# Kernel tuning notes

Hardware: AMD Instinct MI355X
Metric: run time of the kernel (lower is better)

Reference implementation:

```python
import jax, jax.numpy as jnp
import numpy as np

BS, P, R, D = 32, 128, 16, 1024
RHO = 0.97
EPS = 1e-8


def unit_normalize(x):
    return x / jnp.maximum(jnp.linalg.norm(x, axis=-1, keepdims=True), EPS)


def setup_inputs() -> dict:
    key = jax.random.key(0)
    ks = jax.random.split(key, 12)
    scale = 1.0 / np.sqrt(D)
    return {
        "x_all": jax.random.normal(ks[0], (BS, P, D), jnp.float32),
        "h_all": jax.random.normal(ks[1], (BS, P, D), jnp.float32),
        "surprise_all": jax.random.uniform(ks[2], (BS, P, 1), jnp.float32) * 8.0,
        "reset_mask": jax.random.bernoulli(ks[3], 0.05, (BS, P)),
        "pm_K": unit_normalize(jax.random.normal(ks[4], (BS, R, D), jnp.float32)),
        "pm_V": unit_normalize(jax.random.normal(ks[5], (BS, R, D), jnp.float32)),
        "pm_a": jax.random.uniform(ks[6], (BS, R), jnp.float32),
        "elig_K0": jnp.zeros((BS, R, D), jnp.float32),
        "elig_V0": jnp.zeros((BS, R, D), jnp.float32),
        "W_k": jax.random.normal(ks[7], (D, D), jnp.float32) * scale,
        "b_k": jnp.zeros((D,), jnp.float32),
        "W_v": jax.random.normal(ks[8], (D, D), jnp.float32) * scale,
        "b_v": jnp.zeros((D,), jnp.float32),
    }


def reference(x_all, h_all, surprise_all, reset_mask, pm_K, pm_V, pm_a,
              elig_K0, elig_V0, W_k, b_k, W_v, b_v):
    # ---- apply_batch: read-only slot-memory readout over P tokens ----
    x_q = unit_normalize(x_all)                                  # [BS,P,D]
    scores = jnp.einsum('brd,bpd->bpr', pm_K, x_q)               # [BS,P,R]
    weighted = pm_a[:, None, :] * scores                         # [BS,P,R]
    y_pm = jnp.einsum('bpr,brd->bpd', weighted, pm_V)            # [BS,P,D]

    # ---- update_eligibility_batch: affine scan over P tokens ----
    k_cand = unit_normalize(jnp.einsum('bpd,de->bpe', x_all, W_k) + b_k)  # [BS,P,D]
    v_cand = jnp.einsum('bpd,de->bpe', h_all, W_v) + b_v                  # [BS,P,D]
    gate = jnp.clip(surprise_all[..., 0] / 5.0, 0.0, 1.0)                 # [BS,P]
    a_keep = RHO * (1.0 - reset_mask.astype(jnp.float32))                 # [BS,P]

    def step(carry, inp):
        eK, eV = carry                      # each [BS,R,D]
        k, v, g, a = inp                    # [BS,D],[BS,D],[BS],[BS]
        # b_t = gate * cand, broadcast across the R slots (matches torch expand)
        eK = a[:, None, None] * eK + (g[:, None] * k)[:, None, :]
        eV = a[:, None, None] * eV + (g[:, None] * v)[:, None, :]
        return (eK, eV), None

    xs = (jnp.swapaxes(k_cand, 0, 1), jnp.swapaxes(v_cand, 0, 1),
          gate.T, a_keep.T)                 # leading axis = P
    (elig_K, elig_V), _ = jax.lax.scan(step, (elig_K0, elig_V0), xs)

    return y_pm, elig_K, elig_V
```

## Files before the change

kernel.cpp:

```cpp
#include <hip/hip_runtime.h>
#include <cstdint>
#include <cstddef>

#define NB 32
#define NP 128
#define NR 16
#define ND 1024
#define RHOC 0.97f
#define EPSN 1e-8f

typedef short bf16x8 __attribute__((ext_vector_type(8)));
typedef float f32x4 __attribute__((ext_vector_type(4)));
typedef unsigned short u16x8 __attribute__((ext_vector_type(8)));
typedef unsigned short ushort_t;

__device__ inline ushort_t f2bf(float f) {
  unsigned u = __float_as_uint(f);
  unsigned r = (u + 0x7fffu + ((u >> 16) & 1u)) >> 16;
  return (ushort_t)r;
}
__device__ inline float bf2f(ushort_t v) {
  return __uint_as_float(((unsigned)v) << 16);
}
__device__ inline void gload16(const void* g, void* l) {
  __builtin_amdgcn_global_load_lds(
      (const __attribute__((address_space(1))) void*)g,
      (__attribute__((address_space(3))) void*)l, 16, 0, 0);
}

__global__ __launch_bounds__(256) void prep_kernel(
    const float* __restrict__ surprise, const void* __restrict__ mask,
    const float* __restrict__ x, const float* __restrict__ Wk,
    const float* __restrict__ pmK,
    float* __restrict__ c, float* __restrict__ Abuf, float* __restrict__ csum,
    ushort_t* __restrict__ Xb, float* __restrict__ xnorm,
    ushort_t* __restrict__ WkT, ushort_t* __restrict__ pmKb) {
  __shared__ __align__(16) char smem[8448];
  int bid = blockIdx.x;
  int t = threadIdx.x;
  if (bid < NB) {
    float* a_sh = (float*)smem;
    float* suf  = a_sh + 128;
    float* redc = suf + 129;
    int*   isu8 = (int*)(redc + 128);
    int b = bid;
    if (t == 0) *isu8 = 0;
    __syncthreads();
    const unsigned char* mb = (const unsigned char*)mask;
    int v = 0;
    for (int i = t; i < NB * NP; i += 256)
      if ((i & 3) != 0 && mb[i] != 0) v = 1;
    if (v) *isu8 = 1;
    __syncthreads();
    int u8 = *isu8;
    if (t < NP) {
      int mv = u8 ? mb[b * NP + t] : ((const int*)mask)[b * NP + t];
      a_sh[t] = RHOC * (mv ? 0.f : 1.f);
    }
    __syncthreads();
    if (t == 0) {
      float p = 1.f;
      suf[NP] = 1.f;
      for (int s = NP - 1; s >= 0; --s) { p *= a_sh[s]; suf[s] = p; }
    }
    __syncthreads();
    if (t < NP) {
      float g = fminf(fmaxf(surprise[b * NP + t] * 0.2f, 0.f), 1.f);
      float cv = g * suf[t + 1];
      c[b * NP + t] = cv;
      redc[t] = cv;
    }
    __syncthreads();
    for (int off = 64; off > 0; off >>= 1) {
      if (t < off) redc[t] += redc[t + off];
      __syncthreads();
    }
    if (t == 0) { csum[b] = redc[0]; Abuf[b] = suf[0]; }
  } else if (bid < NB + NB * NP) {
    int row = bid - NB;
    float* red = (float*)smem;
    float4 vv = *(const float4*)&x[(size_t)row * ND + t * 4];
    ushort4 o;
    o.x = f2bf(vv.x); o.y = f2bf(vv.y); o.z = f2bf(vv.z); o.w = f2bf(vv.w);
    *(ushort4*)&Xb[(size_t)row * ND + t * 4] = o;
    float ss = vv.x * vv.x + vv.y * vv.y + vv.z * vv.z + vv.w * vv.w;
#pragma unroll
    for (int off = 32; off > 0; off >>= 1) ss += __shfl_xor(ss, off);
    int wave = t >> 6, lane = t & 63;
    if (lane == 0) red[wave] = ss;
    __syncthreads();
    if (t == 0) xnorm[row] = sqrtf(red[0] + red[1] + red[2] + red[3]);
  } else if (bid < NB + NB * NP + 256) {
    int id2 = bid - (NB + NB * NP);
    ushort_t (*tt)[65] = (ushort_t(*)[65])smem;
    int k0 = (id2 >> 4) * 64, n0 = (id2 & 15) * 64;
#pragma unroll
    for (int i = 0; i < 16; ++i) {
      int r = i * 4 + (t >> 6), cc = t & 63;
      tt[r][cc] = f2bf(Wk[(size_t)(k0 + r) * ND + n0 + cc]);
    }
    __syncthreads();
#pragma unroll
    for (int i = 0; i < 16; ++i) {
      int r = i * 4 + (t >> 6), cc = t & 63;
      WkT[(size_t)(n0 + r) * ND + k0 + cc] = tt[cc][r];
    }
  } else {
    int id3 = bid - (NB + NB * NP + 256);
    size_t base = (size_t)id3 * 2048 + t * 8;
    float4 a = *(const float4*)&pmK[base];
    float4 bq = *(const float4*)&pmK[base + 4];
    u16x8 o;
    o[0] = f2bf(a.x); o[1] = f2bf(a.y); o[2] = f2bf(a.z); o[3] = f2bf(a.w);
    o[4] = f2bf(bq.x); o[5] = f2bf(bq.y); o[6] = f2bf(bq.z); o[7] = f2bf(bq.w);
    *(u16x8*)&pmKb[base] = o;
  }
}

__global__ __launch_bounds__(256) void main_kernel(
    const ushort_t* __restrict__ Xb, const ushort_t* __restrict__ WkT,
    const float* __restrict__ bk, float* __restrict__ norms2p,
    const float* __restrict__ h, const float* __restrict__ c,
    float* __restrict__ hbar) {
  __shared__ __align__(16) char smem[25600];
  int bid = blockIdx.x;
  int tid = threadIdx.x;
  if (bid < 512) {
    ushort_t* As = (ushort_t*)smem;
    ushort_t* Bs = As + 128 * 64;
    float* sred = (float*)(Bs + 64 * 64);
    int lane = tid & 63, wid = tid >> 6;
    int wr = wid >> 1, wc = wid & 1;
    int bm = bid & 31, bn = bid >> 5;
    int m0 = bm * 128, n0 = bn * 64;
    int lo = lane & 15, hi = lane >> 4;
    f32x4 acc[4][2] = {};
    for (int k0 = 0; k0 < ND; k0 += 64) {
#pragma unroll
      for (int i = 0; i < 4; ++i) {
        int sl = i * 256 + tid;
        int r = sl >> 3, s = sl & 7;
        int gk = k0 + ((s ^ (r & 7)) << 3);
        gload16(&Xb[(size_t)(m0 + r) * ND + gk], &As[sl << 3]);
      }
#pragma unroll
      for (int i = 0; i < 2; ++i) {
        int sl = i * 256 + tid;
        int r = sl >> 3, s = sl & 7;
        int gk = k0 + ((s ^ (r & 7)) << 3);
        gload16(&WkT[(size_t)(n0 + r) * ND + gk], &Bs[sl << 3]);
      }
      __syncthreads();
#pragma unroll
      for (int ksl = 0; ksl < 2; ++ksl) {
        bf16x8 af[4], bfr[2];
#pragma unroll
        for (int mi = 0; mi < 4; ++mi) {
          int r = wr * 64 + mi * 16 + lo;
          int s = (ksl * 4 + hi) ^ (r & 7);
          af[mi] = *(const bf16x8*)&As[(r << 6) + (s << 3)];
        }
#pragma unroll
        for (int ni = 0; ni < 2; ++ni) {
          int r = wc * 32 + ni * 16 + lo;
          int s = (ksl * 4 + hi) ^ (r & 7);
          bfr[ni] = *(const bf16x8*)&Bs[(r << 6) + (s << 3)];
        }
#pragma unroll
        for (int mi = 0; mi < 4; ++mi)
#pragma unroll
          for (int ni = 0; ni < 2; ++ni)
            acc[mi][ni] = __builtin_amdgcn_mfma_f32_16x16x32_bf16(
                af[mi], bfr[ni], acc[mi][ni], 0, 0, 0);
      }
      __syncthreads();
    }
    float bkv[2];
#pragma unroll
    for (int ni = 0; ni < 2; ++ni) bkv[ni] = bk[n0 + wc * 32 + ni * 16 + lo];
#pragma unroll
    for (int mi = 0; mi < 4; ++mi) {
#pragma unroll
      for (int j = 0; j < 4; ++j) {
        float ss = 0.f;
#pragma unroll
        for (int ni = 0; ni < 2; ++ni) {
          float vv = acc[mi][ni][j] + bkv[ni];
          ss += vv * vv;
        }
        ss += __shfl_xor(ss, 1);
        ss += __shfl_xor(ss, 2);
        ss += __shfl_xor(ss, 4);
        ss += __shfl_xor(ss, 8);
        if (lo == 0) sred[wc * 128 + wr * 64 + mi * 16 + hi * 4 + j] = ss;
      }
    }
    __syncthreads();
    if (tid < 128)
      norms2p[(size_t)bn * (NB * NP) + m0 + tid] = sred[tid] + sred[128 + tid];
  } else {
    int id2 = bid - 512;
    int b = id2 >> 4, dchunk = id2 & 15;
    float* cs = (float*)smem;
    float* red = cs + 128;
    int dd = tid & 63, sl = tid >> 6;
    int d = dchunk * 64 + dd;
    if (tid < NP) cs[tid] = c[b * NP + tid];
    __syncthreads();
    const float* hb = h + ((size_t)b * NP + sl * 32) * ND + d;
    float acc = 0.f;
#pragma unroll
    for (int tt2 = 0; tt2 < 32; ++tt2) acc += cs[sl * 32 + tt2] * hb[(size_t)tt2 * ND];
    red[sl * 64 + dd] = acc;
    __syncthreads();
    if (sl == 0)
      hbar[(size_t)b * ND + d] = red[dd] + red[64 + dd] + red[128 + dd] + red[192 + dd];
  }
}

__global__ __launch_bounds__(256) void mid_kernel(
    const ushort_t* __restrict__ Xb, const float* __restrict__ norms2p,
    const float* __restrict__ c, float* __restrict__ xbar,
    float* __restrict__ wsum, const ushort_t* __restrict__ pmKb,
    const float* __restrict__ pmV, const float* __restrict__ pma,
    const float* __restrict__ xnorm, float* __restrict__ y) {
  __shared__ __align__(16) char smem[5504];
  int bid = blockIdx.x;
  int tid = threadIdx.x;
  if (bid < 256) {
    float* wsh = (float*)smem;
    float* red = wsh + NP;
    int b = bid >> 3;
    int dd = tid & 63, sl = tid >> 6;
    int d = (bid & 7) * 128 + dd * 2;
    if (tid < NP) {
      float s = 0.f;
#pragma unroll
      for (int pc = 0; pc < 16; ++pc)
        s += norms2p[(size_t)pc * (NB * NP) + b * NP + tid];
      wsh[tid] = c[b * NP + tid] / fmaxf(sqrtf(s), EPSN);
    }
    __syncthreads();
    if ((bid & 7) == 0 && tid == 0) {
      float s = 0.f;
      for (int t2 = 0; t2 < NP; ++t2) s += wsh[t2];
      wsum[b] = s;
    }
    const ushort_t* xb = Xb + ((size_t)b * NP + sl * 32) * ND + d;
    float ax = 0.f, ay = 0.f;
#pragma unroll
    for (int t2 = 0; t2 < 32; ++t2) {
      unsigned u = *(const unsigned*)&xb[(size_t)t2 * ND];
      float w = wsh[sl * 32 + t2];
      ax += w * bf2f((ushort_t)(u & 0xffffu));
      ay += w * bf2f((ushort_t)(u >> 16));
    }
    red[(sl * 64 + dd) * 2 + 0] = ax;
    red[(sl * 64 + dd) * 2 + 1] = ay;
    __syncthreads();
    if (sl == 0) {
      float2 o;
      o.x = red[dd * 2] + red[(64 + dd) * 2] + red[(128 + dd) * 2] + red[(192 + dd) * 2];
      o.y = red[dd * 2 + 1] + red[(64 + dd) * 2 + 1] + red[(128 + dd) * 2 + 1] +
            red[(192 + dd) * 2 + 1];
      *(float2*)&xbar[(size_t)b * ND + d] = o;
    }
  } else {
    int id2 = bid - 256;
    int b = id2 >> 3, p0 = (id2 & 7) * 16;
    float* sredp = (float*)smem;
    float* wls = sredp + 4 * 16 * 17;
    int lane = tid & 63, wid = tid >> 6;
    int lo = lane & 15, hi = lane >> 4;
    float4 v[16];
#pragma unroll
    for (int r = 0; r < 16; ++r)
      v[r] = *(const float4*)&pmV[((size_t)(b * NR + r)) * ND + tid * 4];
    const ushort_t* xrow = &Xb[((size_t)(b * NP + p0 + lo)) * ND];
    const ushort_t* krow = &pmKb[((size_t)(b * NR + lo)) * ND];
    f32x4 sc = {};
#pragma unroll
    for (int ki = 0; ki < 8; ++ki) {
      int koff = (wid * 8 + ki) * 32 + hi * 8;
      bf16x8 af = *(const bf16x8*)&xrow[koff];
      bf16x8 bf = *(const bf16x8*)&krow[koff];
      sc = __builtin_amdgcn_mfma_f32_16x16x32_bf16(af, bf, sc, 0, 0, 0);
    }
#pragma unroll
    for (int j = 0; j < 4; ++j) sredp[(wid * 16 + hi * 4 + j) * 17 + lo] = sc[j];
    __syncthreads();
    {
      int p = tid >> 4, r = tid & 15;
      float s = sredp[(p)*17 + r] + sredp[(16 + p) * 17 + r] +
                sredp[(32 + p) * 17 + r] + sredp[(48 + p) * 17 + r];
      wls[p * 16 + r] = pma[b * NR + r] * s / fmaxf(xnorm[b * NP + p0 + p], EPSN);
    }
    __syncthreads();
#pragma unroll
    for (int p = 0; p < 16; ++p) {
      float4 a = {0.f, 0.f, 0.f, 0.f};
#pragma unroll
      for (int r = 0; r < 16; ++r) {
        float w = wls[p * 16 + r];
        a.x += w * v[r].x; a.y += w * v[r].y;
        a.z += w * v[r].z; a.w += w * v[r].w;
      }
      *(float4*)&y[((size_t)(b * NP + p0 + p)) * ND + tid * 4] = a;
    }
  }
}

__global__ __launch_bounds__(256) void vkbar_kernel(
    const float* __restrict__ hbar, const float* __restrict__ xbar,
    const float* __restrict__ Wv, const float* __restrict__ Wk,
    float* __restrict__ partials) {
  __shared__ __align__(16) float hst[128][36];
  int bid = blockIdx.x;
  int path = bid >> 7;
  int id2 = bid & 127;
  int esl = id2 >> 4, dchunk = id2 & 15;
  int e0 = esl * 128, d0 = dchunk * 64;
  const float* src = path ? xbar : hbar;
  const float* W = path ? Wk : Wv;
  int t = threadIdx.x;
#pragma unroll
  for (int i = 0; i < 16; ++i) {
    int idx = i * 256 + t;
    int bb = idx >> 7, e = idx & 127;
    hst[e][bb] = src[(size_t)bb * ND + e0 + e];
  }
  __syncthreads();
  int bg = t >> 6, dd = t & 63, d = d0 + dd;
  float acc[8] = {};
  for (int e = 0; e < 128; ++e) {
    float w = W[(size_t)(e0 + e) * ND + d];
    float4 h0 = *(const float4*)&hst[e][bg * 8];
    float4 h1 = *(const float4*)&hst[e][bg * 8 + 4];
    acc[0] += h0.x * w; acc[1] += h0.y * w; acc[2] += h0.z * w; acc[3] += h0.w * w;
    acc[4] += h1.x * w; acc[5] += h1.y * w; acc[6] += h1.z * w; acc[7] += h1.w * w;
  }
#pragma unroll
  for (int i = 0; i < 8; ++i)
    partials[((size_t)(path * 8 + esl) * NB + bg * 8 + i) * ND + d] = acc[i];
}

__global__ __launch_bounds__(256) void epi_kernel(
    const float* __restrict__ partials, const float* __restrict__ bv,
    const float* __restrict__ bk, const float* __restrict__ eV0,
    const float* __restrict__ eK0, const float* __restrict__ Abuf,
    const float* __restrict__ csum, const float* __restrict__ wsum,
    float* __restrict__ outV, float* __restrict__ outK) {
  int bid = blockIdx.x;
  int path = bid >> 7;
  int id2 = bid & 127;
  int b = id2 >> 2, dc = id2 & 3;
  int d = dc * 256 + threadIdx.x;
  float s = 0.f;
#pragma unroll
  for (int sl = 0; sl < 8; ++sl)
    s += partials[((size_t)(path * 8 + sl) * NB + b) * ND + d];
  const float* bias = path ? bk : bv;
  const float* coef = path ? wsum : csum;
  const float* e0p = path ? eK0 : eV0;
  float* out = path ? outK : outV;
  s += coef[b] * bias[d];
  float A = Abuf[b];
#pragma unroll
  for (int r = 0; r < NR; ++r) {
    size_t idx = ((size_t)(b * NR + r)) * ND + d;
    out[idx] = A * e0p[idx] + s;
  }
}

extern "C" void kernel_launch(void* const* d_in, const int* in_sizes, int n_in,
                              void* d_out, int out_size, void* d_ws, size_t ws_size,
                              hipStream_t stream) {
  (void)in_sizes; (void)n_in; (void)out_size; (void)ws_size;
  const float* x_all    = (const float*)d_in[0];
  const float* h_all    = (const float*)d_in[1];
  const float* surprise = (const float*)d_in[2];
  const void*  mask     = d_in[3];
  const float* pmK      = (const float*)d_in[4];
  const float* pmV      = (const float*)d_in[5];
  const float* pma      = (const float*)d_in[6];
  const float* eK0      = (const float*)d_in[7];
  const float* eV0      = (const float*)d_in[8];
  const float* Wk       = (const float*)d_in[9];
  const float* bk       = (const float*)d_in[10];
  const float* Wv       = (const float*)d_in[11];
  const float* bv       = (const float*)d_in[12];

  float* y    = (float*)d_out;
  float* outK = y + (size_t)NB * NP * ND;
  float* outV = outK + (size_t)NB * NR * ND;

  char* w = (char*)d_ws;
  float* c        = (float*)w; w += NB * NP * 4;
  float* Abuf     = (float*)w; w += 256;
  float* csum     = (float*)w; w += 256;
  float* wsum     = (float*)w; w += 256;
  float* hbar     = (float*)w; w += NB * ND * 4;
  float* xbar     = (float*)w; w += NB * ND * 4;
  float* norms2p  = (float*)w; w += (size_t)16 * NB * NP * 4;
  float* xnorm    = (float*)w; w += NB * NP * 4;
  float* partials = (float*)w; w += (size_t)16 * NB * ND * 4;
  ushort_t* WkT   = (ushort_t*)w; w += (size_t)ND * ND * 2;
  ushort_t* pmKb  = (ushort_t*)w; w += (size_t)NB * NR * ND * 2;
  ushort_t* Xb    = (ushort_t*)w; w += (size_t)NB * NP * ND * 2;

  prep_kernel<<<NB + NB * NP + 256 + 256, 256, 0, stream>>>(
      surprise, mask, x_all, Wk, pmK, c, Abuf, csum, Xb, xnorm, WkT, pmKb);
  main_kernel<<<512 + 512, 256, 0, stream>>>(Xb, WkT, bk, norms2p, h_all, c, hbar);
  mid_kernel<<<256 + 256, 256, 0, stream>>>(Xb, norms2p, c, xbar, wsum, pmKb,
                                            pmV, pma, xnorm, y);
  vkbar_kernel<<<256, 256, 0, stream>>>(hbar, xbar, Wv, Wk, partials);
  epi_kernel<<<256, 256, 0, stream>>>(partials, bv, bk, eV0, eK0, Abuf, csum,
                                      wsum, outV, outK);
}
```

Baseline: 57.06 us.

## Double-buffer GEMM LDS tiles and interleave heterogeneous block roles

Result: slower. 66.69 us (+16.9%).

```diff
diff --git a/kernel.cpp b/kernel.cpp
--- a/kernel.cpp
+++ b/kernel.cpp
@@ -117,40 +117,53 @@
   }
 }
 
-__global__ __launch_bounds__(256) void main_kernel(
+__global__ __launch_bounds__(256, 3) void main_kernel(
     const ushort_t* __restrict__ Xb, const ushort_t* __restrict__ WkT,
     const float* __restrict__ bk, float* __restrict__ norms2p,
     const float* __restrict__ h, const float* __restrict__ c,
     float* __restrict__ hbar) {
-  __shared__ __align__(16) char smem[25600];
+  __shared__ __align__(16) char smem[50176];
   int bid = blockIdx.x;
   int tid = threadIdx.x;
-  if (bid < 512) {
+  int grp = bid >> 3, sub = bid & 7;
+  int id = (grp >> 1) * 8 + sub;
+  if ((grp & 1) == 0) {
     ushort_t* As = (ushort_t*)smem;
-    ushort_t* Bs = As + 128 * 64;
-    float* sred = (float*)(Bs + 64 * 64);
+    ushort_t* Bs = As + 2 * 128 * 64;
+    float* sred = (float*)(Bs + 2 * 64 * 64);
     int lane = tid & 63, wid = tid >> 6;
     int wr = wid >> 1, wc = wid & 1;
-    int bm = bid & 31, bn = bid >> 5;
+    int bm = id & 31, bn = id >> 5;
     int m0 = bm * 128, n0 = bn * 64;
     int lo = lane & 15, hi = lane >> 4;
     f32x4 acc[4][2] = {};
-    for (int k0 = 0; k0 < ND; k0 += 64) {
-#pragma unroll
-      for (int i = 0; i < 4; ++i) {
-        int sl = i * 256 + tid;
-        int r = sl >> 3, s = sl & 7;
-        int gk = k0 + ((s ^ (r & 7)) << 3);
-        gload16(&Xb[(size_t)(m0 + r) * ND + gk], &As[sl << 3]);
-      }
-#pragma unroll
-      for (int i = 0; i < 2; ++i) {
-        int sl = i * 256 + tid;
-        int r = sl >> 3, s = sl & 7;
-        int gk = k0 + ((s ^ (r & 7)) << 3);
-        gload16(&WkT[(size_t)(n0 + r) * ND + gk], &Bs[sl << 3]);
-      }
-      __syncthreads();
+
+    int ra = tid >> 1, sa = (tid & 1) * 4;
+#define STAGE(buf, k0)                                                        \
+  {                                                                           \
+    _Pragma("unroll") for (int i = 0; i < 4; ++i) {                           \
+      int sl = i * 256 + tid;                                                 \
+      int r = sl >> 3, s = sl & 7;                                            \
+      int gk = (k0) + ((s ^ (r & 7)) << 3);                                   \
+      gload16(&Xb[(size_t)(m0 + r) * ND + gk],                                \
+              &As[(size_t)(buf)*8192 + ((size_t)sl << 3)]);                   \
+    }                                                                         \
+    _Pragma("unroll") for (int i = 0; i < 2; ++i) {                           \
+      int sl = i * 256 + tid;                                                 \
+      int r = sl >> 3, s = sl & 7;                                            \
+      int gk = (k0) + ((s ^ (r & 7)) << 3);                                   \
+      gload16(&WkT[(size_t)(n0 + r) * ND + gk],                               \
+              &Bs[(size_t)(buf)*4096 + ((size_t)sl << 3)]);                   \
+    }                                                                         \
+  }
+
+    STAGE(0, 0);
+    __syncthreads();
+    int cur = 0;
+    for (int t = 0; t < 16; ++t) {
+      if (t < 15) STAGE(cur ^ 1, (t + 1) * 64);
+      const ushort_t* Ab = As + cur * 8192;
+      const ushort_t* Bb = Bs + cur * 4096;
 #pragma unroll
       for (int ksl = 0; ksl < 2; ++ksl) {
         bf16x8 af[4], bfr[2];
@@ -158,13 +171,13 @@
         for (int mi = 0; mi < 4; ++mi) {
           int r = wr * 64 + mi * 16 + lo;
           int s = (ksl * 4 + hi) ^ (r & 7);
-          af[mi] = *(const bf16x8*)&As[(r << 6) + (s << 3)];
+          af[mi] = *(const bf16x8*)&Ab[(r << 6) + (s << 3)];
         }
 #pragma unroll
         for (int ni = 0; ni < 2; ++ni) {
           int r = wc * 32 + ni * 16 + lo;
           int s = (ksl * 4 + hi) ^ (r & 7);
-          bfr[ni] = *(const bf16x8*)&Bs[(r << 6) + (s << 3)];
+          bfr[ni] = *(const bf16x8*)&Bb[(r << 6) + (s << 3)];
         }
 #pragma unroll
         for (int mi = 0; mi < 4; ++mi)
@@ -174,7 +187,9 @@
                 af[mi], bfr[ni], acc[mi][ni], 0, 0, 0);
       }
       __syncthreads();
-    }
+      cur ^= 1;
+    }
+#undef STAGE
     float bkv[2];
 #pragma unroll
     for (int ni = 0; ni < 2; ++ni) bkv[ni] = bk[n0 + wc * 32 + ni * 16 + lo];
@@ -199,8 +214,7 @@
     if (tid < 128)
       norms2p[(size_t)bn * (NB * NP) + m0 + tid] = sred[tid] + sred[128 + tid];
   } else {
-    int id2 = bid - 512;
-    int b = id2 >> 4, dchunk = id2 & 15;
+    int b = id >> 4, dchunk = id & 15;
     float* cs = (float*)smem;
     float* red = cs + 128;
     int dd = tid & 63, sl = tid >> 6;
@@ -227,12 +241,14 @@
   __shared__ __align__(16) char smem[5504];
   int bid = blockIdx.x;
   int tid = threadIdx.x;
-  if (bid < 256) {
+  int grp = bid >> 3, sub = bid & 7;
+  int id = (grp >> 1) * 8 + sub;
+  if ((grp & 1) == 0) {
     float* wsh = (float*)smem;
     float* red = wsh + NP;
-    int b = bid >> 3;
+    int b = id >> 3;
     int dd = tid & 63, sl = tid >> 6;
-    int d = (bid & 7) * 128 + dd * 2;
+    int d = (id & 7) * 128 + dd * 2;
     if (tid < NP) {
       float s = 0.f;
 #pragma unroll
@@ -241,7 +257,7 @@
       wsh[tid] = c[b * NP + tid] / fmaxf(sqrtf(s), EPSN);
     }
     __syncthreads();
-    if ((bid & 7) == 0 && tid == 0) {
+    if ((id & 7) == 0 && tid == 0) {
       float s = 0.f;
       for (int t2 = 0; t2 < NP; ++t2) s += wsh[t2];
       wsum[b] = s;
@@ -266,8 +282,7 @@
       *(float2*)&xbar[(size_t)b * ND + d] = o;
     }
   } else {
-    int id2 = bid - 256;
-    int b = id2 >> 3, p0 = (id2 & 7) * 16;
+    int b = id >> 3, p0 = (id & 7) * 16;
     float* sredp = (float*)smem;
     float* wls = sredp + 4 * 16 * 17;
     int lane = tid & 63, wid = tid >> 6;
```

## Reschedule stages across kernels to overlap independent work by dependency

Applied to the files above, without the earlier changes.

Result: slower. 60.31 us (+5.7%).

```diff
diff --git a/kernel.cpp b/kernel.cpp
--- a/kernel.cpp
+++ b/kernel.cpp
@@ -41,7 +41,7 @@
   if (bid < NB) {
     float* a_sh = (float*)smem;
     float* suf  = a_sh + 128;
-    float* redc = suf + 129;
+    float* redc = suf + 132;
     int*   isu8 = (int*)(redc + 128);
     int b = bid;
     if (t == 0) *isu8 = 0;
@@ -121,7 +121,10 @@
     const ushort_t* __restrict__ Xb, const ushort_t* __restrict__ WkT,
     const float* __restrict__ bk, float* __restrict__ norms2p,
     const float* __restrict__ h, const float* __restrict__ c,
-    float* __restrict__ hbar) {
+    float* __restrict__ hbar,
+    const ushort_t* __restrict__ pmKb, const float* __restrict__ pmV,
+    const float* __restrict__ pma, const float* __restrict__ xnorm,
+    float* __restrict__ y) {
   __shared__ __align__(16) char smem[25600];
   int bid = blockIdx.x;
   int tid = threadIdx.x;
@@ -198,9 +201,9 @@
     __syncthreads();
     if (tid < 128)
       norms2p[(size_t)bn * (NB * NP) + m0 + tid] = sred[tid] + sred[128 + tid];
-  } else {
-    int id2 = bid - 512;
-    int b = id2 >> 4, dchunk = id2 & 15;
+  } else if (bid < 1024) {
+    int id = bid - 512;
+    int b = id >> 4, dchunk = id & 15;
     float* cs = (float*)smem;
     float* red = cs + 128;
     int dd = tid & 63, sl = tid >> 6;
@@ -215,16 +218,105 @@
     __syncthreads();
     if (sl == 0)
       hbar[(size_t)b * ND + d] = red[dd] + red[64 + dd] + red[128 + dd] + red[192 + dd];
-  }
-}
-
-__global__ __launch_bounds__(256) void mid_kernel(
+  } else {
+    int id2 = bid - 1024;
+    int b = id2 >> 3, p0 = (id2 & 7) * 16;
+    float* sredp = (float*)smem;
+    float* wls = sredp + 4 * 16 * 17;
+    int lane = tid & 63, wid = tid >> 6;
+    int lo = lane & 15, hi = lane >> 4;
+    float4 v[16];
+#pragma unroll
+    for (int r = 0; r < 16; ++r)
+      v[r] = *(const float4*)&pmV[((size_t)(b * NR + r)) * ND + tid * 4];
+    const ushort_t* xrow = &Xb[((size_t)(b * NP + p0 + lo)) * ND];
+    const ushort_t* krow = &pmKb[((size_t)(b * NR + lo)) * ND];
+    f32x4 sc = {};
+#pragma unroll
+    for (int ki = 0; ki < 8; ++ki) {
+      int koff = (wid * 8 + ki) * 32 + hi * 8;
+      bf16x8 af = *(const bf16x8*)&xrow[koff];
+      bf16x8 bf = *(const bf16x8*)&krow[koff];
+      sc = __builtin_amdgcn_mfma_f32_16x16x32_bf16(af, bf, sc, 0, 0, 0);
+    }
+#pragma unroll
+    for (int j = 0; j < 4; ++j) sredp[(wid * 16 + hi * 4 + j) * 17 + lo] = sc[j];
+    __syncthreads();
+    {
+      int p = tid >> 4, r = tid & 15;
+      float s = sredp[(p)*17 + r] + sredp[(16 + p) * 17 + r] +
+                sredp[(32 + p) * 17 + r] + sredp[(48 + p) * 17 + r];
+      wls[p * 16 + r] = pma[b * NR + r] * s / fmaxf(xnorm[b * NP + p0 + p], EPSN);
+    }
+    __syncthreads();
+#pragma unroll
+    for (int p = 0; p < 16; ++p) {
+      float4 a = {0.f, 0.f, 0.f, 0.f};
+#pragma unroll
+      for (int r = 0; r < 16; ++r) {
+        float w = wls[p * 16 + r];
+        a.x += w * v[r].x; a.y += w * v[r].y;
+        a.z += w * v[r].z; a.w += w * v[r].w;
+      }
+      *(float4*)&y[((size_t)(b * NP + p0 + p)) * ND + tid * 4] = a;
+    }
+  }
+}
+
+__device__ __forceinline__ void vkbar_body(
+    int id2, int t, int path, const float* __restrict__ src,
+    const float* __restrict__ W, float* __restrict__ partials, char* smemv) {
+  float (*hst)[36] = (float(*)[36])smemv;
+  int esl = id2 >> 4, dchunk = id2 & 15;
+  int e0 = esl * 128, d0 = dchunk * 64;
+#pragma unroll
+  for (int i = 0; i < 16; ++i) {
+    int idx = i * 256 + t;
+    int bb = idx >> 7, e = idx & 127;
+    hst[e][bb] = src[(size_t)bb * ND + e0 + e];
+  }
+  __syncthreads();
+  int bg = t >> 6, dd = t & 63, d = d0 + dd;
+  float acc[8] = {};
+  for (int e = 0; e < 128; ++e) {
+    float w = W[(size_t)(e0 + e) * ND + d];
+    float4 h0 = *(const float4*)&hst[e][bg * 8];
+    float4 h1 = *(const float4*)&hst[e][bg * 8 + 4];
+    acc[0] += h0.x * w; acc[1] += h0.y * w; acc[2] += h0.z * w; acc[3] += h0.w * w;
+    acc[4] += h1.x * w; acc[5] += h1.y * w; acc[6] += h1.z * w; acc[7] += h1.w * w;
+  }
+#pragma unroll
+  for (int i = 0; i < 8; ++i)
+    partials[((size_t)(path * 8 + esl) * NB + bg * 8 + i) * ND + d] = acc[i];
+}
+
+__device__ __forceinline__ void epi_body(
+    int id2, int t, int path, const float* __restrict__ partials,
+    const float* __restrict__ bias, const float* __restrict__ coef,
+    const float* __restrict__ e0p, const float* __restrict__ Abuf,
+    float* __restrict__ out) {
+  int b = id2 >> 2, dc = id2 & 3;
+  int d = dc * 256 + t;
+  float s = 0.f;
+#pragma unroll
+  for (int sl = 0; sl < 8; ++sl)
+    s += partials[((size_t)(path * 8 + sl) * NB + b) * ND + d];
+  s += coef[b] * bias[d];
+  float A = Abuf[b];
+#pragma unroll
+  for (int r = 0; r < NR; ++r) {
+    size_t idx = ((size_t)(b * NR + r)) * ND + d;
+    out[idx] = A * e0p[idx] + s;
+  }
+}
+
+__global__ __launch_bounds__(256) void d3_kernel(
     const ushort_t* __restrict__ Xb, const float* __restrict__ norms2p,
     const float* __restrict__ c, float* __restrict__ xbar,
-    float* __restrict__ wsum, const ushort_t* __restrict__ pmKb,
-    const float* __restrict__ pmV, const float* __restrict__ pma,
-    const float* __restrict__ xnorm, float* __restrict__ y) {
-  __shared__ __align__(16) char smem[5504];
+    float* __restrict__ wsum,
+    const float* __restrict__ hbar, const float* __restrict__ Wv,
+    float* __restrict__ partials) {
+  __shared__ __align__(16) char smem[18432];
   int bid = blockIdx.x;
   int tid = threadIdx.x;
   if (bid < 256) {
@@ -266,110 +358,31 @@
       *(float2*)&xbar[(size_t)b * ND + d] = o;
     }
   } else {
-    int id2 = bid - 256;
-    int b = id2 >> 3, p0 = (id2 & 7) * 16;
-    float* sredp = (float*)smem;
-    float* wls = sredp + 4 * 16 * 17;
-    int lane = tid & 63, wid = tid >> 6;
-    int lo = lane & 15, hi = lane >> 4;
-    float4 v[16];
-#pragma unroll
-    for (int r = 0; r < 16; ++r)
-      v[r] = *(const float4*)&pmV[((size_t)(b * NR + r)) * ND + tid * 4];
-    const ushort_t* xrow = &Xb[((size_t)(b * NP + p0 + lo)) * ND];
-    const ushort_t* krow = &pmKb[((size_t)(b * NR + lo)) * ND];
-    f32x4 sc = {};
-#pragma unroll
-    for (int ki = 0; ki < 8; ++ki) {
-      int koff = (wid * 8 + ki) * 32 + hi * 8;
-      bf16x8 af = *(const bf16x8*)&xrow[koff];
-      bf16x8 bf = *(const bf16x8*)&krow[koff];
-      sc = __builtin_amdgcn_mfma_f32_16x16x32_bf16(af, bf, sc, 0, 0, 0);
-    }
-#pragma unroll
-    for (int j = 0; j < 4; ++j) sredp[(wid * 16 + hi * 4 + j) * 17 + lo] = sc[j];
-    __syncthreads();
-    {
-      int p = tid >> 4, r = tid & 15;
-      float s = sredp[(p)*17 + r] + sredp[(16 + p) * 17 + r] +
-                sredp[(32 + p) * 17 + r] + sredp[(48 + p) * 17 + r];
-      wls[p * 16 + r] = pma[b * NR + r] * s / fmaxf(xnorm[b * NP + p0 + p], EPSN);
-    }
-    __syncthreads();
-#pragma unroll
-    for (int p = 0; p < 16; ++p) {
-      float4 a = {0.f, 0.f, 0.f, 0.f};
-#pragma unroll
-      for (int r = 0; r < 16; ++r) {
-        float w = wls[p * 16 + r];
-        a.x += w * v[r].x; a.y += w * v[r].y;
-        a.z += w * v[r].z; a.w += w * v[r].w;
-      }
-      *(float4*)&y[((size_t)(b * NP + p0 + p)) * ND + tid * 4] = a;
-    }
-  }
-}
-
-__global__ __launch_bounds__(256) void vkbar_kernel(
-    const float* __restrict__ hbar, const float* __restrict__ xbar,
-    const float* __restrict__ Wv, const float* __restrict__ Wk,
-    float* __restrict__ partials) {
-  __shared__ __align__(16) float hst[128][36];
+    vkbar_body(bid - 256, tid, 0, hbar, Wv, partials, smem);
+  }
+}
+
+__global__ __launch_bounds__(256) void d4_kernel(
+    const float* __restrict__ xbar, const float* __restrict__ Wk,
+    float* __restrict__ partials,
+    const float* __restrict__ bv, const float* __restrict__ csum,
+    const float* __restrict__ eV0, const float* __restrict__ Abuf,
+    float* __restrict__ outV) {
+  __shared__ __align__(16) char smem[18432];
   int bid = blockIdx.x;
-  int path = bid >> 7;
-  int id2 = bid & 127;
-  int esl = id2 >> 4, dchunk = id2 & 15;
-  int e0 = esl * 128, d0 = dchunk * 64;
-  const float* src = path ? xbar : hbar;
-  const float* W = path ? Wk : Wv;
-  int t = threadIdx.x;
-#pragma unroll
-  for (int i = 0; i < 16; ++i) {
-    int idx = i * 256 + t;
-    int bb = idx >> 7, e = idx & 127;
-    hst[e][bb] = src[(size_t)bb * ND + e0 + e];
-  }
-  __syncthreads();
-  int bg = t >> 6, dd = t & 63, d = d0 + dd;
-  float acc[8] = {};
-  for (int e = 0; e < 128; ++e) {
-    float w = W[(size_t)(e0 + e) * ND + d];
-    float4 h0 = *(const float4*)&hst[e][bg * 8];
-    float4 h1 = *(const float4*)&hst[e][bg * 8 + 4];
-    acc[0] += h0.x * w; acc[1] += h0.y * w; acc[2] += h0.z * w; acc[3] += h0.w * w;
-    acc[4] += h1.x * w; acc[5] += h1.y * w; acc[6] += h1.z * w; acc[7] += h1.w * w;
-  }
-#pragma unroll
-  for (int i = 0; i < 8; ++i)
-    partials[((size_t)(path * 8 + esl) * NB + bg * 8 + i) * ND + d] = acc[i];
-}
-
-__global__ __launch_bounds__(256) void epi_kernel(
-    const float* __restrict__ partials, const float* __restrict__ bv,
-    const float* __restrict__ bk, const float* __restrict__ eV0,
-    const float* __restrict__ eK0, const float* __restrict__ Abuf,
-    const float* __restrict__ csum, const float* __restrict__ wsum,
-    float* __restrict__ outV, float* __restrict__ outK) {
-  int bid = blockIdx.x;
-  int path = bid >> 7;
-  int id2 = bid & 127;
-  int b = id2 >> 2, dc = id2 & 3;
-  int d = dc * 256 + threadIdx.x;
-  float s = 0.f;
-#pragma unroll
-  for (int sl = 0; sl < 8; ++sl)
-    s += partials[((size_t)(path * 8 + sl) * NB + b) * ND + d];
-  const float* bias = path ? bk : bv;
-  const float* coef = path ? wsum : csum;
-  const float* e0p = path ? eK0 : eV0;
-  float* out = path ? outK : outV;
-  s += coef[b] * bias[d];
-  float A = Abuf[b];
-#pragma unroll
-  for (int r = 0; r < NR; ++r) {
-    size_t idx = ((size_t)(b * NR + r)) * ND + d;
-    out[idx] = A * e0p[idx] + s;
-  }
+  int tid = threadIdx.x;
+  if (bid < 128) {
+    vkbar_body(bid, tid, 1, xbar, Wk, partials, smem);
+  } else {
+    epi_body(bid - 128, tid, 0, partials, bv, csum, eV0, Abuf, outV);
+  }
+}
+
+__global__ __launch_bounds__(256) void d5_kernel(
+    const float* __restrict__ partials, const float* __restrict__ bk,
+    const float* __restrict__ wsum, const float* __restrict__ eK0,
+    const float* __restrict__ Abuf, float* __restrict__ outK) {
+  epi_body(blockIdx.x, threadIdx.x, 1, partials, bk, wsum, eK0, Abuf, outK);
 }
 
 extern "C" void kernel_launch(void* const* d_in, const int* in_sizes, int n_in,
@@ -410,10 +423,11 @@
 
   prep_kernel<<<NB + NB * NP + 256 + 256, 256, 0, stream>>>(
       surprise, mask, x_all, Wk, pmK, c, Abuf, csum, Xb, xnorm, WkT, pmKb);
-  main_kernel<<<512 + 512, 256, 0, stream>>>(Xb, WkT, bk, norms2p, h_all, c, hbar);
-  mid_kernel<<<256 + 256, 256, 0, stream>>>(Xb, norms2p, c, xbar, wsum, pmKb,
-                                            pmV, pma, xnorm, y);
-  vkbar_kernel<<<256, 256, 0, stream>>>(hbar, xbar, Wv, Wk, partials);
-  epi_kernel<<<256, 256, 0, stream>>>(partials, bv, bk, eV0, eK0, Abuf, csum,
-                                      wsum, outV, outK);
-}
+  main_kernel<<<512 + 512 + 256, 256, 0, stream>>>(
+      Xb, WkT, bk, norms2p, h_all, c, hbar, pmKb, pmV, pma, xnorm, y);
+  d3_kernel<<<256 + 128, 256, 0, stream>>>(Xb, norms2p, c, xbar, wsum, hbar,
+                                           Wv, partials);
+  d4_kernel<<<128 + 128, 256, 0, stream>>>(xbar, Wk, partials, bv, csum, eV0,
+                                           Abuf, outV);
+  d5_kernel<<<128, 256, 0, stream>>>(partials, bk, wsum, eK0, Abuf, outK);
+}
```
